# Optimization experiments

Measured on AMD Instinct MI355X. Metric: run time of the kernel, lower is better.

Reference implementation:

```python
import jax, jax.numpy as jnp
import numpy as np

DN = ('NCDHW', 'OIDHW', 'NCDHW')
HIDDEN = 512
VOCAB = 8192


def conv3d_s122(x, w, b):
    # stride (1,2,2), padding 1 on all three spatial-temporal dims
    y = jax.lax.conv_general_dilated(x, w, window_strides=(1, 2, 2),
                                     padding=[(1, 1), (1, 1), (1, 1)],
                                     dimension_numbers=DN)
    return y + b[None, :, None, None, None]


def setup_inputs() -> dict:
    key = jax.random.key(0)
    ks = jax.random.split(key, 9)
    c1, c2 = HIDDEN // 4, HIDDEN // 2
    inp = {
        'video': jax.random.normal(ks[0], (2, 3, 16, 128, 128), dtype=jnp.float32),
        'w1': jax.random.normal(ks[1], (c1, 3, 3, 3, 3), dtype=jnp.float32) * 0.05,
        'b1': jnp.zeros((c1,), dtype=jnp.float32),
        'w2': jax.random.normal(ks[2], (c2, c1, 3, 3, 3), dtype=jnp.float32) * 0.05,
        'b2': jnp.zeros((c2,), dtype=jnp.float32),
        'w3': jax.random.normal(ks[3], (HIDDEN, c2, 3, 3, 3), dtype=jnp.float32) * 0.05,
        'b3': jnp.zeros((HIDDEN,), dtype=jnp.float32),
        'codebook': jax.random.normal(ks[4], (VOCAB, HIDDEN), dtype=jnp.float32),
        'emb_table': jax.random.normal(ks[5], (VOCAB, HIDDEN), dtype=jnp.float32),
        'resolution_level': 0,
    }
    return inp


def reference(video, w1, b1, w2, b2, w3, b3, codebook, emb_table, resolution_level):
    h = jax.nn.relu(conv3d_s122(video, w1, b1))
    h = jax.nn.relu(conv3d_s122(h, w2, b2))
    f = conv3d_s122(h, w3, b3)                       # [B, C, T, H', W']
    B, C = f.shape[0], f.shape[1]
    feats = f.reshape(B, C, -1).transpose(0, 2, 1)   # [B, N, C]
    # squared L2 distances (argmin identical to cdist's sqrt distances)
    f2 = jnp.sum(feats * feats, axis=-1, keepdims=True)          # [B, N, 1]
    c2 = jnp.sum(codebook * codebook, axis=-1)                   # [V]
    dots = jnp.einsum('bnc,vc->bnv', feats, codebook)            # [B, N, V]
    sqdist = f2 + c2[None, None, :] - 2.0 * dots
    tokens = jnp.argmin(sqdist, axis=-1)                         # [B, N] int
    embeddings = emb_table[tokens]                               # [B, N, C]
    return tokens, embeddings
```

## Files before the change

### kernel.cpp

```cpp
#include <hip/hip_runtime.h>

typedef __bf16 bf16x8 __attribute__((ext_vector_type(8)));
typedef float  f32x4  __attribute__((ext_vector_type(4)));

__device__ __forceinline__ unsigned int splitpack(float x) {
  unsigned int u = __float_as_uint(x);
  unsigned int hi = (u + 0x7fffu + ((u >> 16) & 1u)) >> 16;
  float l = x - __uint_as_float(hi << 16);
  unsigned int ul = __float_as_uint(l);
  unsigned int lo = (ul + 0x7fffu + ((ul >> 16) & 1u)) >> 16;
  return hi | (lo << 16);
}

__device__ __forceinline__ void mfma_bf16(f32x4& d, uint4 a, uint4 b) {
  d = __builtin_amdgcn_mfma_f32_16x16x32_bf16(
        __builtin_bit_cast(bf16x8, a), __builtin_bit_cast(bf16x8, b), d, 0, 0, 0);
}

__global__ void conv1_k(const float* __restrict__ in, const float* __restrict__ wgt,
                        const float* __restrict__ bias, unsigned int* __restrict__ h1p) {
  const int tx = threadIdx.x;
  const int w0 = tx * 4;
  const int h  = blockIdx.x * 16 + threadIdx.y;
  const int co0 = blockIdx.y * 8;
  const int bz = blockIdx.z;
  const int b = bz >> 4, t = bz & 15;

  float acc[8][4];
  #pragma unroll
  for (int i = 0; i < 8; ++i) {
    const float bv = bias[co0 + i];
    #pragma unroll
    for (int j = 0; j < 4; ++j) acc[i][j] = bv;
  }
  const int cs = 2 * w0 - 2;

  for (int ci = 0; ci < 3; ++ci) {
    const float* inc = in + (size_t)((b * 3 + ci) * 16) * (128 * 128);
    const float* wc  = wgt + ((size_t)co0 * 3 + ci) * 27;
    #pragma unroll
    for (int kd = 0; kd < 3; ++kd) {
      const int t2 = t - 1 + kd;
      if (t2 < 0 || t2 >= 16) continue;
      const float* ip = inc + t2 * (128 * 128);
      #pragma unroll
      for (int kh = 0; kh < 3; ++kh) {
        const int hh = 2 * h - 1 + kh;
        float v[10];
        if (hh >= 0) {
          const float* r = ip + hh * 128 + cs;
          if (cs >= 0) { float2 u = *(const float2*)r; v[0] = u.x; v[1] = u.y; }
          else         { v[0] = 0.f; v[1] = 0.f; }
          float2 u1 = *(const float2*)(r + 2); v[2] = u1.x; v[3] = u1.y;
          float2 u2 = *(const float2*)(r + 4); v[4] = u2.x; v[5] = u2.y;
          float2 u3 = *(const float2*)(r + 6); v[6] = u3.x; v[7] = u3.y;
          float2 u4 = *(const float2*)(r + 8); v[8] = u4.x; v[9] = u4.y;
        } else {
          #pragma unroll
          for (int z = 0; z < 10; ++z) v[z] = 0.f;
        }
        #pragma unroll
        for (int i = 0; i < 8; ++i) {
          const float* wp = wc + (size_t)i * (3 * 27) + kd * 9 + kh * 3;
          const float wa = wp[0], wb = wp[1], wcc = wp[2];
          #pragma unroll
          for (int wi = 0; wi < 4; ++wi) {
            acc[i][wi] = fmaf(v[1 + 2*wi], wa,  acc[i][wi]);
            acc[i][wi] = fmaf(v[2 + 2*wi], wb,  acc[i][wi]);
            acc[i][wi] = fmaf(v[3 + 2*wi], wcc, acc[i][wi]);
          }
        }
      }
    }
  }
  const int ph = h & 1, rr = h >> 1, cc0 = tx * 2;
  #pragma unroll
  for (int i = 0; i < 8; ++i) {
    unsigned int p0 = splitpack(fmaxf(acc[i][0], 0.f));
    unsigned int p1 = splitpack(fmaxf(acc[i][1], 0.f));
    unsigned int p2 = splitpack(fmaxf(acc[i][2], 0.f));
    unsigned int p3 = splitpack(fmaxf(acc[i][3], 0.f));
    const size_t base = ((size_t)((b * 128 + co0 + i) * 16 + t)) * 4096 + ph * 2048 + rr * 32 + cc0;
    *(uint2*)(h1p + base)        = make_uint2(p0, p2);
    *(uint2*)(h1p + base + 1024) = make_uint2(p1, p3);
  }
}

__global__ void split_w2_k(const float* __restrict__ w2, unsigned short* __restrict__ whi,
                           unsigned short* __restrict__ wlo) {
  unsigned int o = blockIdx.x * 256u + threadIdx.x;
  unsigned int j   = o & 7u;
  unsigned int col = (o >> 3) & 127u;
  unsigned int kg  = (o >> 10) & 3u;
  unsigned int cbk = (o >> 12) & 1u;
  unsigned int cic = (o >> 13) & 3u;
  unsigned int tap = o >> 15;
  unsigned int co = cbk * 128u + col, ci = cic * 32u + kg * 8u + j;
  float x = w2[((size_t)co * 128u + ci) * 27u + tap];
  unsigned int p = splitpack(x);
  whi[o] = (unsigned short)(p & 0xffffu);
  wlo[o] = (unsigned short)(p >> 16);
}

__global__ void split_w3_k(const float* __restrict__ w3, unsigned short* __restrict__ whi,
                           unsigned short* __restrict__ wlo) {
  unsigned int o = blockIdx.x * 256u + threadIdx.x;
  unsigned int j   = o & 7u;
  unsigned int col = (o >> 3) & 127u;
  unsigned int kg  = (o >> 10) & 3u;
  unsigned int cb  = (o >> 12) & 3u;
  unsigned int cic = (o >> 14) & 7u;
  unsigned int tap = o >> 17;
  unsigned int co = cb * 128u + col, ci = cic * 32u + kg * 8u + j;
  float x = w3[((size_t)co * 256u + ci) * 27u + tap];
  unsigned int p = splitpack(x);
  whi[o] = (unsigned short)(p & 0xffffu);
  wlo[o] = (unsigned short)(p >> 16);
}

__global__ void split_cb_k(const float* __restrict__ cb, unsigned short* __restrict__ cbhi,
                           unsigned short* __restrict__ cblo) {
  unsigned int o = blockIdx.x * 256u + threadIdx.x;
  unsigned int j   = o & 7u;
  unsigned int row = (o >> 3) & 127u;
  unsigned int kq  = (o >> 10) & 3u;
  unsigned int kc  = (o >> 12) & 15u;
  unsigned int vb  = o >> 16;
  unsigned int v = vb * 128u + row, k = kc * 32u + kq * 8u + j;
  float x = cb[(size_t)v * 512u + k];
  unsigned int p = splitpack(x);
  cbhi[o] = (unsigned short)(p & 0xffffu);
  cblo[o] = (unsigned short)(p >> 16);
}

__global__ void c2_k(const float* __restrict__ cb, float* __restrict__ c2) {
  const int wid = threadIdx.x >> 6, lane = threadIdx.x & 63;
  const int v = blockIdx.x * 4 + wid;
  const float* row = cb + (size_t)v * 512 + lane * 8;
  float4 a = *(const float4*)row, b = *(const float4*)(row + 4);
  float s = a.x*a.x + a.y*a.y + a.z*a.z + a.w*a.w
          + b.x*b.x + b.y*b.y + b.z*b.z + b.w*b.w;
  #pragma unroll
  for (int off = 32; off; off >>= 1) s += __shfl_down(s, off);
  if (lane == 0) c2[v] = s;
}

#define NCH2 108
__global__ __launch_bounds__(512) void conv2_mfma_k(
    const unsigned int* __restrict__ xp,
    const unsigned short* __restrict__ whi, const unsigned short* __restrict__ wlo,
    const float* __restrict__ bias,
    unsigned int* __restrict__ h2p) {
  __shared__ __align__(16) unsigned short lds[16384];

  const int tid  = threadIdx.x;
  const int lane = tid & 63;
  const int wid  = tid >> 6;
  const int wm   = wid >> 2, wn = wid & 3;
  const int cbk = blockIdx.x;
  const int nb  = blockIdx.y;
  const int bt  = blockIdx.z;
  const int b = bt >> 4, t = bt & 15;

  const int skg = tid >> 7;
  const int sn  = tid & 127;
  const int s_hout = nb * 4 + (sn >> 5);
  const int s_wout = sn & 31;
  const int base_ci = b * 8388608 + skg * 524288;

  const int lc = lane & 15, kgl = lane >> 4;
  const uint4* pAhi[4]; const uint4* pAlo[4];
  #pragma unroll
  for (int mf = 0; mf < 4; ++mf) {
    const int off = kgl * 1024 + (wm * 64 + mf * 16 + lc) * 8;
    pAhi[mf] = (const uint4*)&lds[off];
    pAlo[mf] = (const uint4*)&lds[4096 + off];
  }
  const uint4* pBhi[2]; const uint4* pBlo[2];
  #pragma unroll
  for (int nf = 0; nf < 2; ++nf) {
    const int off = kgl * 1024 + (wn * 32 + nf * 16 + lc) * 8;
    pBhi[nf] = (const uint4*)&lds[8192 + off];
    pBlo[nf] = (const uint4*)&lds[12288 + off];
  }
  uint4* wAhi = (uint4*)&lds[tid * 8];
  uint4* wAlo = (uint4*)&lds[4096 + tid * 8];
  uint4* wBhi = (uint4*)&lds[8192  + (skg * 128 + sn) * 8];
  uint4* wBlo = (uint4*)&lds[12288 + (skg * 128 + sn) * 8];

  f32x4 acc[4][2];
  #pragma unroll
  for (int mf = 0; mf < 4; ++mf)
    #pragma unroll
    for (int nf = 0; nf < 2; ++nf) acc[mf][nf] = (f32x4)(0.f);

  uint4 avh, avl;
  unsigned int vals[8];

  auto issue = [&](int ic) {
    const int tap = ic >> 2, cic = ic & 3;
    const int kd = tap / 9, r9 = tap % 9;
    const int kh = r9 / 3, kw = r9 % 3;
    const int tt = t + kd - 1;
    const int pl = ((kh != 1) ? 2 : 0) + ((kw != 1) ? 1 : 0);
    const int r  = s_hout + (kh != 0) - 1;
    const int c  = s_wout + (kw != 0) - 1;
    const bool oob = (tt < 0) || (tt > 15) || (r < 0) || (c < 0);
    const int idx0 = base_ci + cic * 2097152 + tt * 4096 + pl * 1024 + r * 32 + c;
    #pragma unroll
    for (int j = 0; j < 8; ++j) {
      unsigned int sidx = oob ? 0u : (unsigned int)(idx0 + j * 65536);
      unsigned int v = xp[sidx];
      vals[j] = oob ? 0u : v;
    }
    const size_t slab = ((size_t)((tap * 4 + cic) * 2 + cbk)) << 12;
    avh = *(const uint4*)(whi + slab + tid * 8);
    avl = *(const uint4*)(wlo + slab + tid * 8);
  };

  issue(0);

  for (int ic = 0; ic < NCH2; ++ic) {
    __syncthreads();
    *wAhi = avh;
    *wAlo = avl;
    uint4 H, L;
    H.x = (vals[0] & 0xffffu) | (vals[1] << 16);  L.x = (vals[0] >> 16) | (vals[1] & 0xffff0000u);
    H.y = (vals[2] & 0xffffu) | (vals[3] << 16);  L.y = (vals[2] >> 16) | (vals[3] & 0xffff0000u);
    H.z = (vals[4] & 0xffffu) | (vals[5] << 16);  L.z = (vals[4] >> 16) | (vals[5] & 0xffff0000u);
    H.w = (vals[6] & 0xffffu) | (vals[7] << 16);  L.w = (vals[6] >> 16) | (vals[7] & 0xffff0000u);
    *wBhi = H;
    *wBlo = L;
    __syncthreads();
    if (ic + 1 < NCH2) issue(ic + 1);

    uint4 ah[4], al[4], bh[2], bl[2];
    #pragma unroll
    for (int mf = 0; mf < 4; ++mf) { ah[mf] = *pAhi[mf]; al[mf] = *pAlo[mf]; }
    #pragma unroll
    for (int nf = 0; nf < 2; ++nf) { bh[nf] = *pBhi[nf]; bl[nf] = *pBlo[nf]; }

    #pragma unroll
    for (int mf = 0; mf < 4; ++mf)
      #pragma unroll
      for (int nf = 0; nf < 2; ++nf) mfma_bf16(acc[mf][nf], ah[mf], bh[nf]);
    #pragma unroll
    for (int mf = 0; mf < 4; ++mf)
      #pragma unroll
      for (int nf = 0; nf < 2; ++nf) mfma_bf16(acc[mf][nf], ah[mf], bl[nf]);
    #pragma unroll
    for (int mf = 0; mf < 4; ++mf)
      #pragma unroll
      for (int nf = 0; nf < 2; ++nf) mfma_bf16(acc[mf][nf], al[mf], bh[nf]);
  }

  const int lr4 = (lane >> 4) * 4;
  #pragma unroll
  for (int mf = 0; mf < 4; ++mf) {
    const int co0g = cbk * 128 + wm * 64 + mf * 16 + lr4;
    const float4 bv = *(const float4*)(bias + co0g);
    #pragma unroll
    for (int nf = 0; nf < 2; ++nf) {
      const int n_l = wn * 32 + nf * 16 + lc;
      const int h_out = nb * 4 + (n_l >> 5);
      const int w_out = n_l & 31;
      const int pl_o = ((h_out & 1) << 1) | (w_out & 1);
      const size_t sp = pl_o * 256 + (h_out >> 1) * 16 + (w_out >> 1);
      const float* bp = (const float*)&bv;
      #pragma unroll
      for (int r = 0; r < 4; ++r) {
        const int co = co0g + r;
        const float x = fmaxf(acc[mf][nf][r] + bp[r], 0.f);
        h2p[((size_t)((b * 256 + co) * 16 + t)) * 1024 + sp] = splitpack(x);
      }
    }
  }
}

#define NCH 216
__global__ __launch_bounds__(512) void conv3_mfma_k(
    const unsigned int* __restrict__ xp,
    const unsigned short* __restrict__ whi, const unsigned short* __restrict__ wlo,
    const float* __restrict__ bias,
    unsigned short* __restrict__ fhi, unsigned short* __restrict__ flo) {
  __shared__ __align__(16) unsigned short lds[16384];

  const int tid  = threadIdx.x;
  const int lane = tid & 63;
  const int wid  = tid >> 6;
  const int wm   = wid >> 2, wn = wid & 3;
  const int cb = blockIdx.x;
  const int hb = blockIdx.y;
  const int bt = blockIdx.z;
  const int b = bt >> 4, t = bt & 15;

  const int skg = tid >> 7;
  const int sn  = tid & 127;
  const int shn = hb * 8 + (sn >> 4);
  const int swn = sn & 15;
  const int base_ci = b * 4194304 + skg * 131072;

  const int lc = lane & 15, kgl = lane >> 4;
  const uint4* pAhi[4]; const uint4* pAlo[4];
  #pragma unroll
  for (int mf = 0; mf < 4; ++mf) {
    const int off = kgl * 1024 + (wm * 64 + mf * 16 + lc) * 8;
    pAhi[mf] = (const uint4*)&lds[off];
    pAlo[mf] = (const uint4*)&lds[4096 + off];
  }
  const uint4* pBhi[2]; const uint4* pBlo[2];
  #pragma unroll
  for (int nf = 0; nf < 2; ++nf) {
    const int off = kgl * 1024 + (wn * 32 + nf * 16 + lc) * 8;
    pBhi[nf] = (const uint4*)&lds[8192 + off];
    pBlo[nf] = (const uint4*)&lds[12288 + off];
  }
  uint4* wAhi = (uint4*)&lds[tid * 8];
  uint4* wAlo = (uint4*)&lds[4096 + tid * 8];
  uint4* wBhi = (uint4*)&lds[8192  + (skg * 128 + sn) * 8];
  uint4* wBlo = (uint4*)&lds[12288 + (skg * 128 + sn) * 8];

  f32x4 acc[4][2];
  #pragma unroll
  for (int mf = 0; mf < 4; ++mf)
    #pragma unroll
    for (int nf = 0; nf < 2; ++nf) acc[mf][nf] = (f32x4)(0.f);

  uint4 avh, avl;
  unsigned int vals[8];

  auto issue = [&](int ic) {
    const int tap = ic >> 3, cic = ic & 7;
    const int kd = tap / 9, r9 = tap % 9;
    const int kh = r9 / 3, kw = r9 % 3;
    const int tt = t + kd - 1;
    const int pl = ((kh != 1) ? 2 : 0) + ((kw != 1) ? 1 : 0);
    const int r  = shn + (kh != 0) - 1;
    const int c  = swn + (kw != 0) - 1;
    const bool oob = (tt < 0) || (tt > 15) || (r < 0) || (c < 0);
    const int idx0 = base_ci + cic * 524288 + tt * 1024 + pl * 256 + r * 16 + c;
    #pragma unroll
    for (int j = 0; j < 8; ++j) {
      unsigned int sidx = oob ? 0u : (unsigned int)(idx0 + j * 16384);
      unsigned int v = xp[sidx];
      vals[j] = oob ? 0u : v;
    }
    const size_t slab = ((size_t)((tap * 8 + cic) * 4 + cb)) << 12;
    avh = *(const uint4*)(whi + slab + tid * 8);
    avl = *(const uint4*)(wlo + slab + tid * 8);
  };

  issue(0);

  for (int ic = 0; ic < NCH; ++ic) {
    __syncthreads();
    *wAhi = avh;
    *wAlo = avl;
    uint4 H, L;
    H.x = (vals[0] & 0xffffu) | (vals[1] << 16);  L.x = (vals[0] >> 16) | (vals[1] & 0xffff0000u);
    H.y = (vals[2] & 0xffffu) | (vals[3] << 16);  L.y = (vals[2] >> 16) | (vals[3] & 0xffff0000u);
    H.z = (vals[4] & 0xffffu) | (vals[5] << 16);  L.z = (vals[4] >> 16) | (vals[5] & 0xffff0000u);
    H.w = (vals[6] & 0xffffu) | (vals[7] << 16);  L.w = (vals[6] >> 16) | (vals[7] & 0xffff0000u);
    *wBhi = H;
    *wBlo = L;
    __syncthreads();
    if (ic + 1 < NCH) issue(ic + 1);

    uint4 ah[4], al[4], bh[2], bl[2];
    #pragma unroll
    for (int mf = 0; mf < 4; ++mf) { ah[mf] = *pAhi[mf]; al[mf] = *pAlo[mf]; }
    #pragma unroll
    for (int nf = 0; nf < 2; ++nf) { bh[nf] = *pBhi[nf]; bl[nf] = *pBlo[nf]; }

    #pragma unroll
    for (int mf = 0; mf < 4; ++mf)
      #pragma unroll
      for (int nf = 0; nf < 2; ++nf) mfma_bf16(acc[mf][nf], ah[mf], bh[nf]);
    #pragma unroll
    for (int mf = 0; mf < 4; ++mf)
      #pragma unroll
      for (int nf = 0; nf < 2; ++nf) mfma_bf16(acc[mf][nf], ah[mf], bl[nf]);
    #pragma unroll
    for (int mf = 0; mf < 4; ++mf)
      #pragma unroll
      for (int nf = 0; nf < 2; ++nf) mfma_bf16(acc[mf][nf], al[mf], bh[nf]);
  }

  const int lr4 = (lane >> 4) * 4;
  const int tokb = b * 32 + t * 2 + hb;
  #pragma unroll
  for (int mf = 0; mf < 4; ++mf) {
    const int co0g = cb * 128 + wm * 64 + mf * 16 + lr4;
    const float4 bv = *(const float4*)(bias + co0g);
    const int kc = co0g >> 5, kq = (co0g >> 3) & 3, j0 = co0g & 7;
    #pragma unroll
    for (int nf = 0; nf < 2; ++nf) {
      const int n_l = wn * 32 + nf * 16 + lc;
      const size_t off = (size_t)(tokb * 16 + kc) * 4096 + kq * 1024 + n_l * 8 + j0;
      unsigned int p0 = splitpack(acc[mf][nf][0] + bv.x);
      unsigned int p1 = splitpack(acc[mf][nf][1] + bv.y);
      unsigned int p2 = splitpack(acc[mf][nf][2] + bv.z);
      unsigned int p3 = splitpack(acc[mf][nf][3] + bv.w);
      ushort4 h4, l4;
      h4.x = (unsigned short)(p0 & 0xffffu); l4.x = (unsigned short)(p0 >> 16);
      h4.y = (unsigned short)(p1 & 0xffffu); l4.y = (unsigned short)(p1 >> 16);
      h4.z = (unsigned short)(p2 & 0xffffu); l4.z = (unsigned short)(p2 >> 16);
      h4.w = (unsigned short)(p3 & 0xffffu); l4.w = (unsigned short)(p3 >> 16);
      *(ushort4*)(fhi + off) = h4;
      *(ushort4*)(flo + off) = l4;
    }
  }
}

__global__ __launch_bounds__(512) void vq_mfma_k(
    const unsigned short* __restrict__ fhi, const unsigned short* __restrict__ flo,
    const unsigned short* __restrict__ cbhi, const unsigned short* __restrict__ cblo,
    const float* __restrict__ c2,
    float* __restrict__ pval, int* __restrict__ pidx) {
  __shared__ __align__(16) unsigned short lds[16384];

  const int tid  = threadIdx.x;
  const int lane = tid & 63;
  const int wid  = tid >> 6;
  const int wm   = wid >> 2, wn = wid & 3;
  const int vb = blockIdx.x;
  const int tb = blockIdx.y;
  const int v0 = vb * 128, tok0 = tb * 128;

  const int lc = lane & 15, kgl = lane >> 4;
  const uint4* pAhi[4]; const uint4* pAlo[4];
  #pragma unroll
  for (int mf = 0; mf < 4; ++mf) {
    const int off = kgl * 1024 + (wm * 64 + mf * 16 + lc) * 8;
    pAhi[mf] = (const uint4*)&lds[off];
    pAlo[mf] = (const uint4*)&lds[4096 + off];
  }
  const uint4* pBhi[2]; const uint4* pBlo[2];
  #pragma unroll
  for (int nf = 0; nf < 2; ++nf) {
    const int off = kgl * 1024 + (wn * 32 + nf * 16 + lc) * 8;
    pBhi[nf] = (const uint4*)&lds[8192 + off];
    pBlo[nf] = (const uint4*)&lds[12288 + off];
  }
  uint4* wAhi = (uint4*)&lds[tid * 8];
  uint4* wAlo = (uint4*)&lds[4096 + tid * 8];
  uint4* wBhi = (uint4*)&lds[8192 + tid * 8];
  uint4* wBlo = (uint4*)&lds[12288 + tid * 8];

  f32x4 acc[4][2];
  #pragma unroll
  for (int mf = 0; mf < 4; ++mf)
    #pragma unroll
    for (int nf = 0; nf < 2; ++nf) acc[mf][nf] = (f32x4)(0.f);

  uint4 cah, cal, fbh, fbl;
  auto issue = [&](int kc) {
    const size_t cboff = (size_t)(vb * 16 + kc) * 4096 + tid * 8;
    const size_t foff  = (size_t)(tb * 16 + kc) * 4096 + tid * 8;
    cah = *(const uint4*)(cbhi + cboff);
    cal = *(const uint4*)(cblo + cboff);
    fbh = *(const uint4*)(fhi + foff);
    fbl = *(const uint4*)(flo + foff);
  };

  issue(0);

  for (int kc = 0; kc < 16; ++kc) {
    __syncthreads();
    *wAhi = cah;
    *wAlo = cal;
    *wBhi = fbh;
    *wBlo = fbl;
    __syncthreads();
    if (kc + 1 < 16) issue(kc + 1);

    uint4 ah[4], al[4], bh[2], bl[2];
    #pragma unroll
    for (int mf = 0; mf < 4; ++mf) { ah[mf] = *pAhi[mf]; al[mf] = *pAlo[mf]; }
    #pragma unroll
    for (int nf = 0; nf < 2; ++nf) { bh[nf] = *pBhi[nf]; bl[nf] = *pBlo[nf]; }

    #pragma unroll
    for (int mf = 0; mf < 4; ++mf)
      #pragma unroll
      for (int nf = 0; nf < 2; ++nf) mfma_bf16(acc[mf][nf], ah[mf], bh[nf]);
    #pragma unroll
    for (int mf = 0; mf < 4; ++mf)
      #pragma unroll
      for (int nf = 0; nf < 2; ++nf) mfma_bf16(acc[mf][nf], ah[mf], bl[nf]);
    #pragma unroll
    for (int mf = 0; mf < 4; ++mf)
      #pragma unroll
      for (int nf = 0; nf < 2; ++nf) mfma_bf16(acc[mf][nf], al[mf], bh[nf]);
  }

  float best[2]; int bidx[2];
  best[0] = best[1] = 3.4e38f; bidx[0] = bidx[1] = 0;
  #pragma unroll
  for (int mf = 0; mf < 4; ++mf) {
    float cc[4];
    *(float4*)cc = *(const float4*)(c2 + v0 + wm * 64 + mf * 16 + kgl * 4);
    #pragma unroll
    for (int nf = 0; nf < 2; ++nf) {
      #pragma unroll
      for (int r = 0; r < 4; ++r) {
        const float d = cc[r] - 2.f * acc[mf][nf][r];
        const int vg = v0 + wm * 64 + mf * 16 + kgl * 4 + r;
        if (d < best[nf] || (d == best[nf] && vg < bidx[nf])) { best[nf] = d; bidx[nf] = vg; }
      }
    }
  }
  #pragma unroll
  for (int off = 16; off <= 32; off <<= 1) {
    #pragma unroll
    for (int nf = 0; nf < 2; ++nf) {
      const float ov = __shfl_xor(best[nf], off);
      const int   oi = __shfl_xor(bidx[nf], off);
      if (ov < best[nf] || (ov == best[nf] && oi < bidx[nf])) { best[nf] = ov; bidx[nf] = oi; }
    }
  }
  if (lane < 16) {
    #pragma unroll
    for (int nf = 0; nf < 2; ++nf) {
      const int tok = tok0 + wn * 32 + nf * 16 + lane;
      const int slot = vb * 2 + wm;
      pval[(size_t)tok * 128 + slot] = best[nf];
      pidx[(size_t)tok * 128 + slot] = bidx[nf];
    }
  }
}

__global__ void vq_reduce_k(const float* __restrict__ pval, const int* __restrict__ pidx,
                            int* __restrict__ tokens, float* __restrict__ out_tok) {
  const int tok = blockIdx.x * blockDim.x + threadIdx.x;
  float best = 3.4e38f; int bi = 0;
  for (int s = 0; s < 128; ++s) {
    const float v = pval[(size_t)tok * 128 + s];
    const int idx = pidx[(size_t)tok * 128 + s];
    if (v < best || (v == best && idx < bi)) { best = v; bi = idx; }
  }
  tokens[tok] = bi;
  out_tok[tok] = (float)bi;
}

__global__ void gather_k(const int* __restrict__ tokens, const float* __restrict__ emb,
                         float* __restrict__ out) {
  const int i = blockIdx.x * blockDim.x + threadIdx.x;
  const int n = i >> 7;
  const int c4 = (i & 127) * 4;
  const int tk = tokens[n];
  float4 v = *(const float4*)(emb + (size_t)tk * 512 + c4);
  *(float4*)(out + (size_t)n * 512 + c4) = v;
}

extern "C" void kernel_launch(void* const* d_in, const int* in_sizes, int n_in,
                              void* d_out, int out_size, void* d_ws, size_t ws_size,
                              hipStream_t stream) {
  const float* video = (const float*)d_in[0];
  const float* w1 = (const float*)d_in[1];
  const float* b1 = (const float*)d_in[2];
  const float* w2 = (const float*)d_in[3];
  const float* b2 = (const float*)d_in[4];
  const float* w3 = (const float*)d_in[5];
  const float* b3 = (const float*)d_in[6];
  const float* cb  = (const float*)d_in[7];
  const float* emb = (const float*)d_in[8];

  float* ws = (float*)d_ws;
  unsigned int* h1p = (unsigned int*)ws;
  unsigned short* fhi = (unsigned short*)(ws);
  unsigned short* flo = (unsigned short*)(ws + 2097152);
  unsigned short* cbhi = (unsigned short*)(ws + 4194304);
  unsigned short* cblo = (unsigned short*)(ws + 6291456);
  float* c2v  = ws + 8388608;
  float* pval = ws + 8396800;
  int*   pidx = (int*)(ws + 9445376);
  int*   tokens = (int*)(ws + 10493952);
  unsigned int* h2p = (unsigned int*)(ws + 16777216);
  unsigned short* w2hi = (unsigned short*)d_out;
  unsigned short* w2lo = w2hi + 884736;
  unsigned short* w3hi = (unsigned short*)d_out;
  unsigned short* w3lo = w3hi + 3538944;
  float* out_tok = (float*)d_out;
  float* out_emb = (float*)d_out + 8192;

  hipLaunchKernelGGL(conv1_k, dim3(4, 16, 32), dim3(16, 16), 0, stream, video, w1, b1, h1p);
  hipLaunchKernelGGL(split_w2_k, dim3(3456), dim3(256), 0, stream, w2, w2hi, w2lo);
  hipLaunchKernelGGL(conv2_mfma_k, dim3(2, 8, 32), dim3(512), 0, stream,
                     h1p, w2hi, w2lo, b2, h2p);
  hipLaunchKernelGGL(split_w3_k, dim3(13824), dim3(256), 0, stream, w3, w3hi, w3lo);
  hipLaunchKernelGGL(split_cb_k, dim3(16384), dim3(256), 0, stream, cb, cbhi, cblo);
  hipLaunchKernelGGL(c2_k, dim3(2048), dim3(256), 0, stream, cb, c2v);
  hipLaunchKernelGGL(conv3_mfma_k, dim3(4, 2, 32), dim3(512), 0, stream,
                     h2p, w3hi, w3lo, b3, fhi, flo);
  hipLaunchKernelGGL(vq_mfma_k, dim3(64, 64), dim3(512), 0, stream,
                     fhi, flo, cbhi, cblo, c2v, pval, pidx);
  hipLaunchKernelGGL(vq_reduce_k, dim3(32), dim3(256), 0, stream, pval, pidx, tokens, out_tok);
  hipLaunchKernelGGL(gather_k, dim3(4096), dim3(256), 0, stream, tokens, emb, out_emb);
}
```

Baseline: 827.4 us.

## Interleave activations channel-innermost and double-buffer LDS in conv2/conv3 MFMA loops

Conv1 and conv2 now write their split-bf16 activations with 8 channels innermost per spatial position. The consumer convolutions can then fetch each 8-channel group with two 16-byte vector loads instead of eight strided scalar loads. The conv2 and conv3 main loops also use two LDS buffers with two chunks prefetched in flight, which removes one barrier per chunk and overlaps global loads with MFMA work. The costs are double the shared memory per block, which may reduce occupancy, and more live registers.

```diff
diff --git a/kernel.cpp b/kernel.cpp
--- a/kernel.cpp
+++ b/kernel.cpp
@@ -16,6 +16,7 @@
   d = __builtin_amdgcn_mfma_f32_16x16x32_bf16(
         __builtin_bit_cast(bf16x8, a), __builtin_bit_cast(bf16x8, b), d, 0, 0, 0);
 }
+
 
 __global__ void conv1_k(const float* __restrict__ in, const float* __restrict__ wgt,
                         const float* __restrict__ bias, unsigned int* __restrict__ h1p) {
@@ -74,15 +75,18 @@
     }
   }
   const int ph = h & 1, rr = h >> 1, cc0 = tx * 2;
+  const size_t base0 = (size_t)b * 8388608 + (size_t)blockIdx.y * 524288
+                     + (size_t)t * 32768 + (size_t)(ph * 2) * 8192 + (size_t)rr * 256;
   #pragma unroll
   for (int i = 0; i < 8; ++i) {
     unsigned int p0 = splitpack(fmaxf(acc[i][0], 0.f));
     unsigned int p1 = splitpack(fmaxf(acc[i][1], 0.f));
     unsigned int p2 = splitpack(fmaxf(acc[i][2], 0.f));
     unsigned int p3 = splitpack(fmaxf(acc[i][3], 0.f));
-    const size_t base = ((size_t)((b * 128 + co0 + i) * 16 + t)) * 4096 + ph * 2048 + rr * 32 + cc0;
-    *(uint2*)(h1p + base)        = make_uint2(p0, p2);
-    *(uint2*)(h1p + base + 1024) = make_uint2(p1, p3);
+    h1p[base0 + cc0 * 8 + i]              = p0;
+    h1p[base0 + 8192 + cc0 * 8 + i]       = p1;
+    h1p[base0 + (cc0 + 1) * 8 + i]        = p2;
+    h1p[base0 + 8192 + (cc0 + 1) * 8 + i] = p3;
   }
 }
 
@@ -146,12 +150,13 @@
 }
 
 #define NCH2 108
+#define BUFO 16384
 __global__ __launch_bounds__(512) void conv2_mfma_k(
     const unsigned int* __restrict__ xp,
     const unsigned short* __restrict__ whi, const unsigned short* __restrict__ wlo,
     const float* __restrict__ bias,
     unsigned int* __restrict__ h2p) {
-  __shared__ __align__(16) unsigned short lds[16384];
+  __shared__ __align__(16) unsigned short lds[32768];
 
   const int tid  = threadIdx.x;
   const int lane = tid & 63;
@@ -166,27 +171,8 @@
   const int sn  = tid & 127;
   const int s_hout = nb * 4 + (sn >> 5);
   const int s_wout = sn & 31;
-  const int base_ci = b * 8388608 + skg * 524288;
 
   const int lc = lane & 15, kgl = lane >> 4;
-  const uint4* pAhi[4]; const uint4* pAlo[4];
-  #pragma unroll
-  for (int mf = 0; mf < 4; ++mf) {
-    const int off = kgl * 1024 + (wm * 64 + mf * 16 + lc) * 8;
-    pAhi[mf] = (const uint4*)&lds[off];
-    pAlo[mf] = (const uint4*)&lds[4096 + off];
-  }
-  const uint4* pBhi[2]; const uint4* pBlo[2];
-  #pragma unroll
-  for (int nf = 0; nf < 2; ++nf) {
-    const int off = kgl * 1024 + (wn * 32 + nf * 16 + lc) * 8;
-    pBhi[nf] = (const uint4*)&lds[8192 + off];
-    pBlo[nf] = (const uint4*)&lds[12288 + off];
-  }
-  uint4* wAhi = (uint4*)&lds[tid * 8];
-  uint4* wAlo = (uint4*)&lds[4096 + tid * 8];
-  uint4* wBhi = (uint4*)&lds[8192  + (skg * 128 + sn) * 8];
-  uint4* wBlo = (uint4*)&lds[12288 + (skg * 128 + sn) * 8];
 
   f32x4 acc[4][2];
   #pragma unroll
@@ -194,10 +180,7 @@
     #pragma unroll
     for (int nf = 0; nf < 2; ++nf) acc[mf][nf] = (f32x4)(0.f);
 
-  uint4 avh, avl;
-  unsigned int vals[8];
-
-  auto issue = [&](int ic) {
+  auto issue = [&](int ic, uint4& xa, uint4& xb, uint4& wh, uint4& wl) {
     const int tap = ic >> 2, cic = ic & 3;
     const int kd = tap / 9, r9 = tap % 9;
     const int kh = r9 / 3, kw = r9 % 3;
@@ -206,52 +189,70 @@
     const int r  = s_hout + (kh != 0) - 1;
     const int c  = s_wout + (kw != 0) - 1;
     const bool oob = (tt < 0) || (tt > 15) || (r < 0) || (c < 0);
-    const int idx0 = base_ci + cic * 2097152 + tt * 4096 + pl * 1024 + r * 32 + c;
-    #pragma unroll
-    for (int j = 0; j < 8; ++j) {
-      unsigned int sidx = oob ? 0u : (unsigned int)(idx0 + j * 65536);
-      unsigned int v = xp[sidx];
-      vals[j] = oob ? 0u : v;
-    }
+    const int o = b * 8388608 + (cic * 4 + skg) * 524288 + tt * 32768 + pl * 8192 + (r * 32 + c) * 8;
+    const unsigned int* src = xp + (oob ? 0 : o);
+    uint4 a = *(const uint4*)src, bb = *(const uint4*)(src + 4);
+    if (oob) { a = make_uint4(0u,0u,0u,0u); bb = make_uint4(0u,0u,0u,0u); }
+    xa = a; xb = bb;
     const size_t slab = ((size_t)((tap * 4 + cic) * 2 + cbk)) << 12;
-    avh = *(const uint4*)(whi + slab + tid * 8);
-    avl = *(const uint4*)(wlo + slab + tid * 8);
-  };
-
-  issue(0);
-
-  for (int ic = 0; ic < NCH2; ++ic) {
+    wh = *(const uint4*)(whi + slab + tid * 8);
+    wl = *(const uint4*)(wlo + slab + tid * 8);
+  };
+
+  auto stage = [&](int bo, const uint4& xa, const uint4& xb, const uint4& wh, const uint4& wl) {
+    *(uint4*)&lds[bo + tid * 8] = wh;
+    *(uint4*)&lds[bo + 4096 + tid * 8] = wl;
+    uint4 H, L;
+    H.x = (xa.x & 0xffffu) | (xa.y << 16);  L.x = (xa.x >> 16) | (xa.y & 0xffff0000u);
+    H.y = (xa.z & 0xffffu) | (xa.w << 16);  L.y = (xa.z >> 16) | (xa.w & 0xffff0000u);
+    H.z = (xb.x & 0xffffu) | (xb.y << 16);  L.z = (xb.x >> 16) | (xb.y & 0xffff0000u);
+    H.w = (xb.z & 0xffffu) | (xb.w << 16);  L.w = (xb.z >> 16) | (xb.w & 0xffff0000u);
+    *(uint4*)&lds[bo + 8192  + (skg * 128 + sn) * 8] = H;
+    *(uint4*)&lds[bo + 12288 + (skg * 128 + sn) * 8] = L;
+  };
+
+  auto mma = [&](int bo) {
+    uint4 ah[4], al[4], bh[2], bl[2];
+    #pragma unroll
+    for (int mf = 0; mf < 4; ++mf) {
+      const int o = bo + kgl * 1024 + (wm * 64 + mf * 16 + lc) * 8;
+      ah[mf] = *(const uint4*)&lds[o];
+      al[mf] = *(const uint4*)&lds[o + 4096];
+    }
+    #pragma unroll
+    for (int nf = 0; nf < 2; ++nf) {
+      const int o = bo + 8192 + kgl * 1024 + (wn * 32 + nf * 16 + lc) * 8;
+      bh[nf] = *(const uint4*)&lds[o];
+      bl[nf] = *(const uint4*)&lds[o + 4096];
+    }
+    #pragma unroll
+    for (int mf = 0; mf < 4; ++mf)
+      #pragma unroll
+      for (int nf = 0; nf < 2; ++nf) mfma_bf16(acc[mf][nf], ah[mf], bh[nf]);
+    #pragma unroll
+    for (int mf = 0; mf < 4; ++mf)
+      #pragma unroll
+      for (int nf = 0; nf < 2; ++nf) mfma_bf16(acc[mf][nf], ah[mf], bl[nf]);
+    #pragma unroll
+    for (int mf = 0; mf < 4; ++mf)
+      #pragma unroll
+      for (int nf = 0; nf < 2; ++nf) mfma_bf16(acc[mf][nf], al[mf], bh[nf]);
+  };
+
+  uint4 xa0, xb0, wh0, wl0, xa1, xb1, wh1, wl1;
+  issue(0, xa0, xb0, wh0, wl0);
+  issue(1, xa1, xb1, wh1, wl1);
+
+  #pragma unroll 1
+  for (int ic = 0; ic < NCH2; ic += 2) {
+    stage(0, xa0, xb0, wh0, wl0);
     __syncthreads();
-    *wAhi = avh;
-    *wAlo = avl;
-    uint4 H, L;
-    H.x = (vals[0] & 0xffffu) | (vals[1] << 16);  L.x = (vals[0] >> 16) | (vals[1] & 0xffff0000u);
-    H.y = (vals[2] & 0xffffu) | (vals[3] << 16);  L.y = (vals[2] >> 16) | (vals[3] & 0xffff0000u);
-    H.z = (vals[4] & 0xffffu) | (vals[5] << 16);  L.z = (vals[4] >> 16) | (vals[5] & 0xffff0000u);
-    H.w = (vals[6] & 0xffffu) | (vals[7] << 16);  L.w = (vals[6] >> 16) | (vals[7] & 0xffff0000u);
-    *wBhi = H;
-    *wBlo = L;
+    if (ic + 2 < NCH2) issue(ic + 2, xa0, xb0, wh0, wl0);
+    mma(0);
+    stage(BUFO, xa1, xb1, wh1, wl1);
     __syncthreads();
-    if (ic + 1 < NCH2) issue(ic + 1);
-
-    uint4 ah[4], al[4], bh[2], bl[2];
-    #pragma unroll
-    for (int mf = 0; mf < 4; ++mf) { ah[mf] = *pAhi[mf]; al[mf] = *pAlo[mf]; }
-    #pragma unroll
-    for (int nf = 0; nf < 2; ++nf) { bh[nf] = *pBhi[nf]; bl[nf] = *pBlo[nf]; }
-
-    #pragma unroll
-    for (int mf = 0; mf < 4; ++mf)
-      #pragma unroll
-      for (int nf = 0; nf < 2; ++nf) mfma_bf16(acc[mf][nf], ah[mf], bh[nf]);
-    #pragma unroll
-    for (int mf = 0; mf < 4; ++mf)
-      #pragma unroll
-      for (int nf = 0; nf < 2; ++nf) mfma_bf16(acc[mf][nf], ah[mf], bl[nf]);
-    #pragma unroll
-    for (int mf = 0; mf < 4; ++mf)
-      #pragma unroll
-      for (int nf = 0; nf < 2; ++nf) mfma_bf16(acc[mf][nf], al[mf], bh[nf]);
+    if (ic + 3 < NCH2) issue(ic + 3, xa1, xb1, wh1, wl1);
+    mma(BUFO);
   }
 
   const int lr4 = (lane >> 4) * 4;
@@ -259,19 +260,19 @@
   for (int mf = 0; mf < 4; ++mf) {
     const int co0g = cbk * 128 + wm * 64 + mf * 16 + lr4;
     const float4 bv = *(const float4*)(bias + co0g);
+    const float* bp = (const float*)&bv;
+    const size_t gbase = (size_t)(b * 32 + (co0g >> 3)) * 131072 + (size_t)t * 8192 + (co0g & 7);
     #pragma unroll
     for (int nf = 0; nf < 2; ++nf) {
       const int n_l = wn * 32 + nf * 16 + lc;
       const int h_out = nb * 4 + (n_l >> 5);
       const int w_out = n_l & 31;
       const int pl_o = ((h_out & 1) << 1) | (w_out & 1);
-      const size_t sp = pl_o * 256 + (h_out >> 1) * 16 + (w_out >> 1);
-      const float* bp = (const float*)&bv;
+      const size_t sp = gbase + (size_t)pl_o * 2048 + (size_t)((h_out >> 1) * 16 + (w_out >> 1)) * 8;
       #pragma unroll
       for (int r = 0; r < 4; ++r) {
-        const int co = co0g + r;
         const float x = fmaxf(acc[mf][nf][r] + bp[r], 0.f);
-        h2p[((size_t)((b * 256 + co) * 16 + t)) * 1024 + sp] = splitpack(x);
+        h2p[sp + r] = splitpack(x);
       }
     }
   }
@@ -283,7 +284,7 @@
     const unsigned short* __restrict__ whi, const unsigned short* __restrict__ wlo,
     const float* __restrict__ bias,
     unsigned short* __restrict__ fhi, unsigned short* __restrict__ flo) {
-  __shared__ __align__(16) unsigned short lds[16384];
+  __shared__ __align__(16) unsigned short lds[32768];
 
   const int tid  = threadIdx.x;
   const int lane = tid & 63;
@@ -298,27 +299,8 @@
   const int sn  = tid & 127;
   const int shn = hb * 8 + (sn >> 4);
   const int swn = sn & 15;
-  const int base_ci = b * 4194304 + skg * 131072;
 
   const int lc = lane & 15, kgl = lane >> 4;
-  const uint4* pAhi[4]; const uint4* pAlo[4];
-  #pragma unroll
-  for (int mf = 0; mf < 4; ++mf) {
-    const int off = kgl * 1024 + (wm * 64 + mf * 16 + lc) * 8;
-    pAhi[mf] = (const uint4*)&lds[off];
-    pAlo[mf] = (const uint4*)&lds[4096 + off];
-  }
-  const uint4* pBhi[2]; const uint4* pBlo[2];
-  #pragma unroll
-  for (int nf = 0; nf < 2; ++nf) {
-    const int off = kgl * 1024 + (wn * 32 + nf * 16 + lc) * 8;
-    pBhi[nf] = (const uint4*)&lds[8192 + off];
-    pBlo[nf] = (const uint4*)&lds[12288 + off];
-  }
-  uint4* wAhi = (uint4*)&lds[tid * 8];
-  uint4* wAlo = (uint4*)&lds[4096 + tid * 8];
-  uint4* wBhi = (uint4*)&lds[8192  + (skg * 128 + sn) * 8];
-  uint4* wBlo = (uint4*)&lds[12288 + (skg * 128 + sn) * 8];
 
   f32x4 acc[4][2];
   #pragma unroll
@@ -326,10 +308,7 @@
     #pragma unroll
     for (int nf = 0; nf < 2; ++nf) acc[mf][nf] = (f32x4)(0.f);
 
-  uint4 avh, avl;
-  unsigned int vals[8];
-
-  auto issue = [&](int ic) {
+  auto issue = [&](int ic, uint4& xa, uint4& xb, uint4& wh, uint4& wl) {
     const int tap = ic >> 3, cic = ic & 7;
     const int kd = tap / 9, r9 = tap % 9;
     const int kh = r9 / 3, kw = r9 % 3;
@@ -338,52 +317,70 @@
     const int r  = shn + (kh != 0) - 1;
     const int c  = swn + (kw != 0) - 1;
     const bool oob = (tt < 0) || (tt > 15) || (r < 0) || (c < 0);
-    const int idx0 = base_ci + cic * 524288 + tt * 1024 + pl * 256 + r * 16 + c;
-    #pragma unroll
-    for (int j = 0; j < 8; ++j) {
-      unsigned int sidx = oob ? 0u : (unsigned int)(idx0 + j * 16384);
-      unsigned int v = xp[sidx];
-      vals[j] = oob ? 0u : v;
-    }
+    const int o = b * 4194304 + (cic * 4 + skg) * 131072 + tt * 8192 + pl * 2048 + (r * 16 + c) * 8;
+    const unsigned int* src = xp + (oob ? 0 : o);
+    uint4 a = *(const uint4*)src, bb = *(const uint4*)(src + 4);
+    if (oob) { a = make_uint4(0u,0u,0u,0u); bb = make_uint4(0u,0u,0u,0u); }
+    xa = a; xb = bb;
     const size_t slab = ((size_t)((tap * 8 + cic) * 4 + cb)) << 12;
-    avh = *(const uint4*)(whi + slab + tid * 8);
-    avl = *(const uint4*)(wlo + slab + tid * 8);
-  };
-
-  issue(0);
-
-  for (int ic = 0; ic < NCH; ++ic) {
+    wh = *(const uint4*)(whi + slab + tid * 8);
+    wl = *(const uint4*)(wlo + slab + tid * 8);
+  };
+
+  auto stage = [&](int bo, const uint4& xa, const uint4& xb, const uint4& wh, const uint4& wl) {
+    *(uint4*)&lds[bo + tid * 8] = wh;
+    *(uint4*)&lds[bo + 4096 + tid * 8] = wl;
+    uint4 H, L;
+    H.x = (xa.x & 0xffffu) | (xa.y << 16);  L.x = (xa.x >> 16) | (xa.y & 0xffff0000u);
+    H.y = (xa.z & 0xffffu) | (xa.w << 16);  L.y = (xa.z >> 16) | (xa.w & 0xffff0000u);
+    H.z = (xb.x & 0xffffu) | (xb.y << 16);  L.z = (xb.x >> 16) | (xb.y & 0xffff0000u);
+    H.w = (xb.z & 0xffffu) | (xb.w << 16);  L.w = (xb.z >> 16) | (xb.w & 0xffff0000u);
+    *(uint4*)&lds[bo + 8192  + (skg * 128 + sn) * 8] = H;
+    *(uint4*)&lds[bo + 12288 + (skg * 128 + sn) * 8] = L;
+  };
+
+  auto mma = [&](int bo) {
+    uint4 ah[4], al[4], bh[2], bl[2];
+    #pragma unroll
+    for (int mf = 0; mf < 4; ++mf) {
+      const int o = bo + kgl * 1024 + (wm * 64 + mf * 16 + lc) * 8;
+      ah[mf] = *(const uint4*)&lds[o];
+      al[mf] = *(const uint4*)&lds[o + 4096];
+    }
+    #pragma unroll
+    for (int nf = 0; nf < 2; ++nf) {
+      const int o = bo + 8192 + kgl * 1024 + (wn * 32 + nf * 16 + lc) * 8;
+      bh[nf] = *(const uint4*)&lds[o];
+      bl[nf] = *(const uint4*)&lds[o + 4096];
+    }
+    #pragma unroll
+    for (int mf = 0; mf < 4; ++mf)
+      #pragma unroll
+      for (int nf = 0; nf < 2; ++nf) mfma_bf16(acc[mf][nf], ah[mf], bh[nf]);
+    #pragma unroll
+    for (int mf = 0; mf < 4; ++mf)
+      #pragma unroll
+      for (int nf = 0; nf < 2; ++nf) mfma_bf16(acc[mf][nf], ah[mf], bl[nf]);
+    #pragma unroll
+    for (int mf = 0; mf < 4; ++mf)
+      #pragma unroll
+      for (int nf = 0; nf < 2; ++nf) mfma_bf16(acc[mf][nf], al[mf], bh[nf]);
+  };
+
+  uint4 xa0, xb0, wh0, wl0, xa1, xb1, wh1, wl1;
+  issue(0, xa0, xb0, wh0, wl0);
+  issue(1, xa1, xb1, wh1, wl1);
+
+  #pragma unroll 1
+  for (int ic = 0; ic < NCH; ic += 2) {
+    stage(0, xa0, xb0, wh0, wl0);
     __syncthreads();
-    *wAhi = avh;
-    *wAlo = avl;
-    uint4 H, L;
-    H.x = (vals[0] & 0xffffu) | (vals[1] << 16);  L.x = (vals[0] >> 16) | (vals[1] & 0xffff0000u);
-    H.y = (vals[2] & 0xffffu) | (vals[3] << 16);  L.y = (vals[2] >> 16) | (vals[3] & 0xffff0000u);
-    H.z = (vals[4] & 0xffffu) | (vals[5] << 16);  L.z = (vals[4] >> 16) | (vals[5] & 0xffff0000u);
-    H.w = (vals[6] & 0xffffu) | (vals[7] << 16);  L.w = (vals[6] >> 16) | (vals[7] & 0xffff0000u);
-    *wBhi = H;
-    *wBlo = L;
+    if (ic + 2 < NCH) issue(ic + 2, xa0, xb0, wh0, wl0);
+    mma(0);
+    stage(BUFO, xa1, xb1, wh1, wl1);
     __syncthreads();
-    if (ic + 1 < NCH) issue(ic + 1);
-
-    uint4 ah[4], al[4], bh[2], bl[2];
-    #pragma unroll
-    for (int mf = 0; mf < 4; ++mf) { ah[mf] = *pAhi[mf]; al[mf] = *pAlo[mf]; }
-    #pragma unroll
-    for (int nf = 0; nf < 2; ++nf) { bh[nf] = *pBhi[nf]; bl[nf] = *pBlo[nf]; }
-
-    #pragma unroll
-    for (int mf = 0; mf < 4; ++mf)
-      #pragma unroll
-      for (int nf = 0; nf < 2; ++nf) mfma_bf16(acc[mf][nf], ah[mf], bh[nf]);
-    #pragma unroll
-    for (int mf = 0; mf < 4; ++mf)
-      #pragma unroll
-      for (int nf = 0; nf < 2; ++nf) mfma_bf16(acc[mf][nf], ah[mf], bl[nf]);
-    #pragma unroll
-    for (int mf = 0; mf < 4; ++mf)
-      #pragma unroll
-      for (int nf = 0; nf < 2; ++nf) mfma_bf16(acc[mf][nf], al[mf], bh[nf]);
+    if (ic + 3 < NCH) issue(ic + 3, xa1, xb1, wh1, wl1);
+    mma(BUFO);
   }
 
   const int lr4 = (lane >> 4) * 4;
```

New measurement: 742.5 us. 10.3% less time.
